# Kernel tuning notes

Hardware: AMD Instinct MI355X
Metric: run time of the kernel (lower is better)

Reference implementation:

```python
import jax, jax.numpy as jnp
import numpy as np

N_NODES = 10000
N_EDGES = 320000
H = 256
L = 3
EPS = 1e-5


def _mlp2(x, w1, b1, w2, b2):
    # Linear -> ReLU -> Linear
    return jax.nn.relu(x @ w1 + b1) @ w2 + b2


def _layer_norm(x, g, b):
    mu = jnp.mean(x, axis=-1, keepdims=True)
    var = jnp.var(x, axis=-1, keepdims=True)
    return (x - mu) * jax.lax.rsqrt(var + EPS) * g + b


def setup_inputs() -> dict:
    key = jax.random.key(0)
    ks = jax.random.split(key, 24)
    s = 0.02
    inp = {
        "node_features": jax.random.normal(ks[0], (N_NODES, H), dtype=jnp.float32),
        "edge_index": jax.random.randint(ks[1], (2, N_EDGES), 0, N_NODES, dtype=jnp.int64),
        # node encoder (Linear 256->256, ReLU, Linear 256->256)
        "ne_w1": jax.random.normal(ks[2], (H, H), dtype=jnp.float32) * s,
        "ne_b1": jnp.zeros((H,), jnp.float32),
        "ne_w2": jax.random.normal(ks[3], (H, H), dtype=jnp.float32) * s,
        "ne_b2": jnp.zeros((H,), jnp.float32),
        # per-layer message MLP (2H->H, ReLU, H->H), stacked over L layers
        "msg_w1": jax.random.normal(ks[4], (L, 2 * H, H), dtype=jnp.float32) * s,
        "msg_b1": jnp.zeros((L, H), jnp.float32),
        "msg_w2": jax.random.normal(ks[5], (L, H, H), dtype=jnp.float32) * s,
        "msg_b2": jnp.zeros((L, H), jnp.float32),
        # per-layer update MLP (2H->H, ReLU, H->H)
        "upd_w1": jax.random.normal(ks[6], (L, 2 * H, H), dtype=jnp.float32) * s,
        "upd_b1": jnp.zeros((L, H), jnp.float32),
        "upd_w2": jax.random.normal(ks[7], (L, H, H), dtype=jnp.float32) * s,
        "upd_b2": jnp.zeros((L, H), jnp.float32),
        # per-layer LayerNorm
        "ln_g": jnp.ones((L, H), jnp.float32),
        "ln_b": jnp.zeros((L, H), jnp.float32),
        # readout MLP
        "ro_w1": jax.random.normal(ks[8], (H, H), dtype=jnp.float32) * s,
        "ro_b1": jnp.zeros((H,), jnp.float32),
        "ro_w2": jax.random.normal(ks[9], (H, H), dtype=jnp.float32) * s,
        "ro_b2": jnp.zeros((H,), jnp.float32),
    }
    return inp


def reference(node_features, edge_index, ne_w1, ne_b1, ne_w2, ne_b2,
              msg_w1, msg_b1, msg_w2, msg_b2,
              upd_w1, upd_b1, upd_w2, upd_b2,
              ln_g, ln_b, ro_w1, ro_b1, ro_w2, ro_b2):
    n_nodes = node_features.shape[0]
    src, dst = edge_index[0], edge_index[1]

    # node encoder
    x = _mlp2(node_features, ne_w1, ne_b1, ne_w2, ne_b2)  # [N, H]

    # message passing layers (edge_attr is unused in the original layer)
    for l in range(L):
        cat_e = jnp.concatenate([x[src], x[dst]], axis=-1)          # [E, 2H]
        messages = _mlp2(cat_e, msg_w1[l], msg_b1[l], msg_w2[l], msg_b2[l])  # [E, H]
        aggregated = jax.ops.segment_sum(messages, dst, num_segments=n_nodes)  # [N, H]
        cat_n = jnp.concatenate([x, aggregated], axis=-1)           # [N, 2H]
        updated = _mlp2(cat_n, upd_w1[l], upd_b1[l], upd_w2[l], upd_b2[l])
        x = _layer_norm(x + updated, ln_g[l], ln_b[l])

    # mean readout
    g = jnp.mean(x, axis=0)  # [H]
    return _mlp2(g, ro_w1, ro_b1, ro_w2, ro_b2)  # [H]
```

## Files before the change

### kernel.cpp

```cpp
#include <hip/hip_runtime.h>

#define NN 10000
#define NE 320000
#define HD 256
#define NL 3

typedef unsigned short ushort_t;
typedef __attribute__((ext_vector_type(8))) short bf16x8;
typedef __attribute__((ext_vector_type(4))) float f32x4;

#define MFMA __builtin_amdgcn_mfma_f32_16x16x32_bf16

#define LGKMBAR() do { asm volatile("s_waitcnt lgkmcnt(0)" ::: "memory"); \
                       __builtin_amdgcn_s_barrier(); __builtin_amdgcn_sched_barrier(0); } while (0)

__device__ __forceinline__ unsigned short f2bf(float x) {
    unsigned u = __float_as_uint(x);
    unsigned rounding = 0x7FFFu + ((u >> 16) & 1u);
    return (unsigned short)((u + rounding) >> 16);
}
__device__ __forceinline__ float bf2f(unsigned short u) {
    return __uint_as_float(((unsigned)u) << 16);
}


__global__ void hist_deg(const int* __restrict__ dst, int* __restrict__ deg, int E) {
    int e = blockIdx.x * blockDim.x + threadIdx.x;
    if (e < E) atomicAdd(&deg[dst[e]], 1);
}

__global__ __launch_bounds__(1024) void scan_csr(const int* __restrict__ deg,
                                                 int* __restrict__ row_start,
                                                 int* __restrict__ cursor,
                                                 float* __restrict__ degf,
                                                 float* __restrict__ gsum, int n) {
    __shared__ int wsum[16];
    __shared__ int carry_s;
    int tid = threadIdx.x, lane = tid & 63, wid = tid >> 6;
    if (tid < HD) gsum[tid] = 0.f;
    if (tid == 0) carry_s = 0;
    __syncthreads();
    for (int base = 0; base < n; base += 1024) {
        int i = base + tid;
        int v = (i < n) ? deg[i] : 0;
        int s = v;
        #pragma unroll
        for (int off = 1; off < 64; off <<= 1) {
            int t = __shfl_up(s, off);
            if (lane >= off) s += t;
        }
        if (lane == 63) wsum[wid] = s;
        __syncthreads();
        if (wid == 0 && lane < 16) {
            int ws = wsum[lane];
            #pragma unroll
            for (int off = 1; off < 16; off <<= 1) {
                int t = __shfl_up(ws, off);
                if (lane >= off) ws += t;
            }
            wsum[lane] = ws;
        }
        __syncthreads();
        int carry = carry_s;
        int wpre = (wid > 0) ? wsum[wid - 1] : 0;
        int incl = carry + wpre + s;
        int excl = incl - v;
        if (i < n) { row_start[i] = excl; cursor[i] = excl; degf[i] = (float)v; }
        __syncthreads();
        if (tid == 1023) carry_s = incl;
        __syncthreads();
    }
    if (tid == 0) row_start[n] = carry_s;
}

__global__ void scatter_src(const int* __restrict__ src, const int* __restrict__ dst,
                            int* __restrict__ cursor, int* __restrict__ src_sorted, int E) {
    int e = blockIdx.x * blockDim.x + threadIdx.x;
    if (e < E) {
        int pos = atomicAdd(&cursor[dst[e]], 1);
        src_sorted[pos] = src[e];
    }
}


struct TDesc { const float* src; ushort_t* dst; int mode; };
struct TArgs { TDesc d[20]; };

__global__ __launch_bounds__(256) void conv_t(TArgs args) {
    __shared__ ushort_t tile[64][65];
    const float* src = args.d[blockIdx.y].src;
    ushort_t* dst = args.d[blockIdx.y].dst;
    int mode = args.d[blockIdx.y].mode;
    int t = blockIdx.x;
    int r0 = (t >> 2) * 64, c0 = (t & 3) * 64;
    int tid = threadIdx.x;
    int rr = tid >> 4, cc4 = (tid & 15) * 4;
    if (mode == 0) {
        #pragma unroll
        for (int i = 0; i < 4; ++i) {
            int r = r0 + rr + i * 16;
            float4 v = *(const float4*)(src + (size_t)r * HD + c0 + cc4);
            ushort4 o = { f2bf(v.x), f2bf(v.y), f2bf(v.z), f2bf(v.w) };
            *(ushort4*)(dst + (size_t)r * HD + c0 + cc4) = o;
        }
        return;
    }
    #pragma unroll
    for (int i = 0; i < 4; ++i) {
        int r = rr + i * 16;
        float4 v = *(const float4*)(src + (size_t)(r0 + r) * HD + c0 + cc4);
        tile[cc4 + 0][r] = f2bf(v.x);
        tile[cc4 + 1][r] = f2bf(v.y);
        tile[cc4 + 2][r] = f2bf(v.z);
        tile[cc4 + 3][r] = f2bf(v.w);
    }
    __syncthreads();
    #pragma unroll
    for (int i = 0; i < 4; ++i) {
        int c = rr + i * 16;
        ushort4 o = { tile[c][cc4], tile[c][cc4 + 1], tile[c][cc4 + 2], tile[c][cc4 + 3] };
        if (mode == 1) {
            *(ushort4*)(dst + (size_t)(c0 + c) * HD + r0 + cc4) = o;
        } else {
            int col = c0 + c;
            int k = r0 + cc4;
            *(ushort4*)(dst + (size_t)(k >> 5) * 8192 + col * 32 + (k & 31)) = o;
        }
    }
}

__global__ __launch_bounds__(256) void cast_nf_tiled(const float* __restrict__ src,
                                                     ushort_t* __restrict__ dst) {
    int blk = blockIdx.x;
    int row = threadIdx.x >> 4, g = threadIdx.x & 15;
    const float* sp = src + ((size_t)blk * 16 + row) * HD + g * 16;
    ushort_t* dp = dst + (size_t)blk * 4096 + (g >> 1) * 512 + row * 32 + (g & 1) * 16;
    #pragma unroll
    for (int j = 0; j < 4; ++j) {
        float4 v = *(const float4*)(sp + j * 4);
        ushort4 o = { f2bf(v.x), f2bf(v.y), f2bf(v.z), f2bf(v.w) };
        *(ushort4*)(dp + j * 4) = o;
    }
}

__global__ __launch_bounds__(256) void bias_compose(const float* __restrict__ mb2,
                                                    const float* __restrict__ uw1,
                                                    float* __restrict__ out) {
    int l = blockIdx.x, c = threadIdx.x;
    const float* b2l = mb2 + (size_t)l * HD;
    const float* u1b = uw1 + (size_t)l * 2 * HD * HD + (size_t)HD * HD;
    float s = 0.f;
    for (int k = 0; k < HD; ++k) s += b2l[k] * u1b[(size_t)k * HD + c];
    out[(size_t)l * HD + c] = s;
}

__global__ __launch_bounds__(256) void gemm_w2u(
    const ushort_t* __restrict__ Abase, const ushort_t* __restrict__ Btbase,
    ushort_t* __restrict__ outBase)
{
    const ushort_t* A  = Abase  + (size_t)blockIdx.z * HD * HD;
    const ushort_t* Bt = Btbase + (size_t)blockIdx.z * HD * HD;
    ushort_t* outB     = outBase + (size_t)blockIdx.z * HD * HD;
    int tid = threadIdx.x;
    int wid = tid >> 6, lane = tid & 63;
    int wm = wid >> 1, wn = wid & 1;
    int row0 = blockIdx.x * 64 + wm * 32;
    int col0 = blockIdx.y * 64 + wn * 32;
    int lm = lane & 15, lk = (lane >> 4) * 8;
    f32x4 acc[2][2] = {};
    const ushort_t* a0p = A + (size_t)(row0 + lm) * HD + lk;
    const ushort_t* a1p = A + (size_t)(row0 + 16 + lm) * HD + lk;
    const ushort_t* b0p = Bt + (size_t)(col0 + lm) * HD + lk;
    const ushort_t* b1p = Bt + (size_t)(col0 + 16 + lm) * HD + lk;
    #pragma unroll
    for (int k0 = 0; k0 < HD; k0 += 32) {
        bf16x8 a0 = *(const bf16x8*)(a0p + k0);
        bf16x8 a1 = *(const bf16x8*)(a1p + k0);
        bf16x8 b0 = *(const bf16x8*)(b0p + k0);
        bf16x8 b1 = *(const bf16x8*)(b1p + k0);
        acc[0][0] = MFMA(a0, b0, acc[0][0], 0, 0, 0);
        acc[0][1] = MFMA(a0, b1, acc[0][1], 0, 0, 0);
        acc[1][0] = MFMA(a1, b0, acc[1][0], 0, 0, 0);
        acc[1][1] = MFMA(a1, b1, acc[1][1], 0, 0, 0);
    }
    int orow = (lane >> 4) * 4;
    #pragma unroll
    for (int mi = 0; mi < 2; ++mi)
        #pragma unroll
        for (int r = 0; r < 4; ++r) {
            int row = row0 + mi * 16 + orow + r;
            #pragma unroll
            for (int ni = 0; ni < 2; ++ni) {
                int col = col0 + ni * 16 + lm;
                outB[(size_t)(col >> 5) * 8192 + row * 32 + (col & 31)] = f2bf(acc[mi][ni][r]);
            }
        }
}

__device__ __forceinline__ int swz(int row, int byte_in_row) {
    return row * 512 + (byte_in_row ^ ((row & 7) << 4));
}


__global__ __launch_bounds__(512, 4) void enc_pq(
    const ushort_t* __restrict__ Anf, const ushort_t* __restrict__ B1t,
    const ushort_t* __restrict__ B2t,
    const float* __restrict__ b1, const float* __restrict__ b2,
    const ushort_t* __restrict__ Pw1t, const ushort_t* __restrict__ Pw1b,
    const float* __restrict__ pqb1,
    float* __restrict__ xF, ushort_t* __restrict__ xB,
    ushort_t* __restrict__ P, float* __restrict__ Q, int M)
{
    __shared__ char hid[16 * 512];
    int tid = threadIdx.x;
    int w = tid >> 6, lane = tid & 63;
    int lm = lane & 15, q = lane >> 4;
    int row0 = blockIdx.x * 16;
    int col0 = w * 32;
    int cA = col0 + lm, cB = col0 + 16 + lm;
    size_t boff = (size_t)(col0 + lm) * 64 + q * 16;

    auto ldW = [&](const ushort_t* Wt, int s, int ni) -> bf16x8 {
        return *(const bf16x8*)((const char*)Wt + (size_t)s * 16384 + boff + ni * 1024);
    };
    const ushort_t* ap = Anf + (size_t)blockIdx.x * 4096 + lm * 32 + q * 8;

    bf16x8 wb[2][2], axr[2];
    #pragma unroll
    for (int s = 0; s < 2; ++s) {
        wb[s][0] = ldW(B1t, s, 0); wb[s][1] = ldW(B1t, s, 1);
        axr[s] = *(const bf16x8*)(ap + s * 512);
    }
    float b1v[2] = { b1[cA], b1[cB] };
    float b2v[2] = { b2[cA], b2[cB] };

    f32x4 acc[2] = {};
    #pragma unroll
    for (int j = 0; j < 8; ++j) {
        int p = j & 1;
        acc[0] = MFMA(axr[p], wb[p][0], acc[0], 0, 0, 0);
        acc[1] = MFMA(axr[p], wb[p][1], acc[1], 0, 0, 0);
        if (j < 6) {
            wb[p][0] = ldW(B1t, j + 2, 0); wb[p][1] = ldW(B1t, j + 2, 1);
            axr[p] = *(const bf16x8*)(ap + (j + 2) * 512);
        }
    }

    bf16x8 vw[2][2];
    #pragma unroll
    for (int s = 0; s < 2; ++s) { vw[s][0] = ldW(B2t, s, 0); vw[s][1] = ldW(B2t, s, 1); }

    #pragma unroll
    for (int ni = 0; ni < 2; ++ni) {
        int col = col0 + 16 * ni + lm;
        #pragma unroll
        for (int r = 0; r < 4; ++r) {
            int row = 4 * q + r;
            float v = fmaxf(acc[ni][r] + b1v[ni], 0.f);
            *(ushort_t*)(hid + swz(row, col * 2)) = f2bf(v);
        }
    }
    LGKMBAR();

    f32x4 acc2[2] = {};
    #pragma unroll
    for (int j = 0; j < 8; ++j) {
        int p = j & 1;
        int bk = (j * 32 + q * 8) * 2;
        bf16x8 a = *(const bf16x8*)(hid + swz(lm, bk));
        acc2[0] = MFMA(a, vw[p][0], acc2[0], 0, 0, 0);
        acc2[1] = MFMA(a, vw[p][1], acc2[1], 0, 0, 0);
        if (j < 6) { vw[p][0] = ldW(B2t, j + 2, 0); vw[p][1] = ldW(B2t, j + 2, 1); }
    }

    bf16x8 pw[2][2], qw[2][2];
    #pragma unroll
    for (int s = 0; s < 2; ++s) {
        pw[s][0] = ldW(Pw1t, s, 0); pw[s][1] = ldW(Pw1t, s, 1);
        qw[s][0] = ldW(Pw1b, s, 0); qw[s][1] = ldW(Pw1b, s, 1);
    }
    float pqv[2] = { pqb1[cA], pqb1[cB] };
    LGKMBAR();
    int tbase = blockIdx.x * 4096 + w * 512;
    #pragma unroll
    for (int ni = 0; ni < 2; ++ni) {
        int col = col0 + 16 * ni + lm;
        #pragma unroll
        for (int r = 0; r < 4; ++r) {
            int row = 4 * q + r;
            int grow = row0 + row;
            float v = acc2[ni][r] + b2v[ni];
            *(ushort_t*)(hid + swz(row, col * 2)) = f2bf(v);
            xF[(size_t)grow * HD + col] = v;
            xB[tbase + row * 32 + 16 * ni + lm] = f2bf(v);
        }
    }
    LGKMBAR();

    f32x4 aP[2] = {}, aQ[2] = {};
    #pragma unroll
    for (int j = 0; j < 8; ++j) {
        int p = j & 1;
        int bk = (j * 32 + q * 8) * 2;
        bf16x8 a = *(const bf16x8*)(hid + swz(lm, bk));
        aP[0] = MFMA(a, pw[p][0], aP[0], 0, 0, 0);
        aP[1] = MFMA(a, pw[p][1], aP[1], 0, 0, 0);
        aQ[0] = MFMA(a, qw[p][0], aQ[0], 0, 0, 0);
        aQ[1] = MFMA(a, qw[p][1], aQ[1], 0, 0, 0);
        if (j < 6) {
            pw[p][0] = ldW(Pw1t, j + 2, 0); pw[p][1] = ldW(Pw1t, j + 2, 1);
            qw[p][0] = ldW(Pw1b, j + 2, 0); qw[p][1] = ldW(Pw1b, j + 2, 1);
        }
    }
    #pragma unroll
    for (int r = 0; r < 4; ++r) {
        int grow = row0 + 4 * q + r;
        #pragma unroll
        for (int ni = 0; ni < 2; ++ni) {
            int col = col0 + 16 * ni + lm;
            P[(size_t)grow * HD + col] = f2bf(aP[ni][r]);
            Q[(size_t)grow * HD + col] = aQ[ni][r] + pqv[ni];
        }
    }
}


__global__ __launch_bounds__(256) void edge_agg(
    const ushort_t* __restrict__ Pb, const float* __restrict__ Qf,
    const int* __restrict__ row_start, const int* __restrict__ srcs,
    ushort_t* __restrict__ HaggT)
{
    int node = blockIdx.x * 4 + (threadIdx.x >> 6);
    int lane = threadIdx.x & 63;
    int c4 = lane * 4;
    float4 qb = *(const float4*)(Qf + (size_t)node * HD + c4);
    float4 acc = {0.f, 0.f, 0.f, 0.f};
    int j = row_start[node], e = row_start[node + 1];
    for (; j + 8 <= e; j += 8) {
        ushort4 p[8];
        #pragma unroll
        for (int u = 0; u < 8; ++u) {
            int s = srcs[j + u];
            p[u] = *(const ushort4*)(Pb + (size_t)s * HD + c4);
        }
        #pragma unroll
        for (int u = 0; u < 8; ++u) {
            acc.x += fmaxf(bf2f(p[u].x) + qb.x, 0.f);
            acc.y += fmaxf(bf2f(p[u].y) + qb.y, 0.f);
            acc.z += fmaxf(bf2f(p[u].z) + qb.z, 0.f);
            acc.w += fmaxf(bf2f(p[u].w) + qb.w, 0.f);
        }
    }
    for (; j < e; ++j) {
        int s0 = srcs[j];
        ushort4 p0 = *(const ushort4*)(Pb + (size_t)s0 * HD + c4);
        acc.x += fmaxf(bf2f(p0.x) + qb.x, 0.f);
        acc.y += fmaxf(bf2f(p0.y) + qb.y, 0.f);
        acc.z += fmaxf(bf2f(p0.z) + qb.z, 0.f);
        acc.w += fmaxf(bf2f(p0.w) + qb.w, 0.f);
    }
    ushort4 o = { f2bf(acc.x), f2bf(acc.y), f2bf(acc.z), f2bf(acc.w) };
    int tidx = (node >> 4) * 4096 + (c4 >> 5) * 512 + (node & 15) * 32 + (c4 & 31);
    *(ushort4*)(HaggT + tidx) = o;
}


__global__ __launch_bounds__(512, 4) void upd_ln(
    const ushort_t* __restrict__ xb, const ushort_t* __restrict__ Hb,
    const ushort_t* __restrict__ B1t, const ushort_t* __restrict__ B2t,
    const ushort_t* __restrict__ B3t,
    const float* __restrict__ degf,
    const float* __restrict__ b1, const float* __restrict__ bias2,
    const float* __restrict__ b3,
    const float* __restrict__ g, const float* __restrict__ bb,
    const ushort_t* __restrict__ Pw1t, const ushort_t* __restrict__ Pw1b,
    const float* __restrict__ pqb1,
    float* __restrict__ gsum,
    float* __restrict__ xF, ushort_t* __restrict__ xB,
    ushort_t* __restrict__ P, float* __restrict__ Q, int M)
{
    __shared__ char hid[16 * 512];
    __shared__ float sS[8][16], sQ[8][16], muv[16], ivv[16];
    int tid = threadIdx.x;
    int w = tid >> 6, lane = tid & 63;
    int lm = lane & 15, q = lane >> 4;
    int row0 = blockIdx.x * 16;
    int col0 = w * 32;
    int cA = col0 + lm, cB = col0 + 16 + lm;
    size_t boff = (size_t)(col0 + lm) * 64 + q * 16;

    auto ldW = [&](const ushort_t* Wt, int s, int ni) -> bf16x8 {
        return *(const bf16x8*)((const char*)Wt + (size_t)s * 16384 + boff + ni * 1024);
    };
    const ushort_t* xp = xb + (size_t)blockIdx.x * 4096 + lm * 32 + q * 8;
    const ushort_t* hp = Hb + (size_t)blockIdx.x * 4096 + lm * 32 + q * 8;

    bf16x8 wb[2][2][2], axr[2], ahr[2];
    #pragma unroll
    for (int s = 0; s < 2; ++s) {
        wb[s][0][0] = ldW(B1t, s, 0); wb[s][0][1] = ldW(B1t, s, 1);
        wb[s][1][0] = ldW(B2t, s, 0); wb[s][1][1] = ldW(B2t, s, 1);
        axr[s] = *(const bf16x8*)(xp + s * 512);
        ahr[s] = *(const bf16x8*)(hp + s * 512);
    }
    float b1v[2] = { b1[cA], b1[cB] };
    float bzv[2] = { bias2[cA], bias2[cB] };
    float dgv[4];
    #pragma unroll
    for (int r = 0; r < 4; ++r) dgv[r] = degf[min(row0 + 4 * q + r, M - 1)];

    f32x4 acc[2] = {};
    #pragma unroll
    for (int j = 0; j < 8; ++j) {
        int p = j & 1;
        acc[0] = MFMA(axr[p], wb[p][0][0], acc[0], 0, 0, 0);
        acc[0] = MFMA(ahr[p], wb[p][1][0], acc[0], 0, 0, 0);
        acc[1] = MFMA(axr[p], wb[p][0][1], acc[1], 0, 0, 0);
        acc[1] = MFMA(ahr[p], wb[p][1][1], acc[1], 0, 0, 0);
        if (j < 6) {
            wb[p][0][0] = ldW(B1t, j + 2, 0); wb[p][0][1] = ldW(B1t, j + 2, 1);
            wb[p][1][0] = ldW(B2t, j + 2, 0); wb[p][1][1] = ldW(B2t, j + 2, 1);
            axr[p] = *(const bf16x8*)(xp + (j + 2) * 512);
            ahr[p] = *(const bf16x8*)(hp + (j + 2) * 512);
        }
    }

    bf16x8 uw[2][2];
    #pragma unroll
    for (int s = 0; s < 2; ++s) { uw[s][0] = ldW(B3t, s, 0); uw[s][1] = ldW(B3t, s, 1); }

    #pragma unroll
    for (int r = 0; r < 4; ++r) {
        int row = 4 * q + r;
        #pragma unroll
        for (int ni = 0; ni < 2; ++ni) {
            int col = col0 + 16 * ni + lm;
            float v = fmaxf(acc[ni][r] + b1v[ni] + dgv[r] * bzv[ni], 0.f);
            *(ushort_t*)(hid + swz(row, col * 2)) = f2bf(v);
        }
    }
    LGKMBAR();

    float b3v[2] = { b3[cA], b3[cB] };
    float gv[2]  = { g[cA],  g[cB]  };
    float bbv[2] = { bb[cA], bb[cB] };
    float res[2][4];
    #pragma unroll
    for (int r = 0; r < 4; ++r) {
        int gr = min(row0 + 4 * q + r, M - 1);
        res[0][r] = xF[(size_t)gr * HD + cA];
        res[1][r] = xF[(size_t)gr * HD + cB];
    }

    f32x4 acc2[2] = {};
    #pragma unroll
    for (int j = 0; j < 8; ++j) {
        int p = j & 1;
        int bk = (j * 32 + q * 8) * 2;
        bf16x8 a = *(const bf16x8*)(hid + swz(lm, bk));
        acc2[0] = MFMA(a, uw[p][0], acc2[0], 0, 0, 0);
        acc2[1] = MFMA(a, uw[p][1], acc2[1], 0, 0, 0);
        if (j < 6) { uw[p][0] = ldW(B3t, j + 2, 0); uw[p][1] = ldW(B3t, j + 2, 1); }
    }

    bf16x8 pw[2][2], qw[2][2];
    float pqv[2] = { 0.f, 0.f };
    if (Pw1t) {
        #pragma unroll
        for (int s = 0; s < 2; ++s) {
            pw[s][0] = ldW(Pw1t, s, 0); pw[s][1] = ldW(Pw1t, s, 1);
            qw[s][0] = ldW(Pw1b, s, 0); qw[s][1] = ldW(Pw1b, s, 1);
        }
        pqv[0] = pqb1[cA]; pqv[1] = pqb1[cB];
    }

    #pragma unroll
    for (int r = 0; r < 4; ++r) {
        float s = 0.f, qq = 0.f;
        #pragma unroll
        for (int ni = 0; ni < 2; ++ni) {
            float v = acc2[ni][r] + b3v[ni] + res[ni][r];
            acc2[ni][r] = v;
            s += v; qq += v * v;
        }
        #pragma unroll
        for (int off = 1; off < 16; off <<= 1) {
            s += __shfl_xor(s, off);
            qq += __shfl_xor(qq, off);
        }
        if (lm == 0) {
            int row = 4 * q + r;
            sS[w][row] = s; sQ[w][row] = qq;
        }
    }
    LGKMBAR();
    if (tid < 16) {
        float s = 0.f, qq = 0.f;
        #pragma unroll
        for (int i = 0; i < 8; ++i) { s += sS[i][tid]; qq += sQ[i][tid]; }
        float mu = s * (1.0f / HD);
        float var = qq * (1.0f / HD) - mu * mu;
        muv[tid] = mu;
        ivv[tid] = rsqrtf(var + 1e-5f);
    }
    LGKMBAR();
    float csum[2] = {0.f, 0.f};
    int tbase = blockIdx.x * 4096 + w * 512;
    #pragma unroll
    for (int r = 0; r < 4; ++r) {
        int row = 4 * q + r;
        int grow = row0 + row;
        float mu = muv[row], iv = ivv[row];
        #pragma unroll
        for (int ni = 0; ni < 2; ++ni) {
            int col = col0 + 16 * ni + lm;
            float o = (acc2[ni][r] - mu) * iv * gv[ni] + bbv[ni];
            *(ushort_t*)(hid + swz(row, col * 2)) = f2bf(o);
            xF[(size_t)grow * HD + col] = o;
            xB[tbase + row * 32 + 16 * ni + lm] = f2bf(o);
            csum[ni] += o;
        }
    }
    if (gsum) {
        #pragma unroll
        for (int ni = 0; ni < 2; ++ni) {
            float s = csum[ni];
            s += __shfl_xor(s, 16);
            s += __shfl_xor(s, 32);
            if (q == 0) atomicAdd(&gsum[col0 + 16 * ni + lm], s);
        }
    }

    if (Pw1t) {
        LGKMBAR();
        f32x4 aP[2] = {}, aQ[2] = {};
        #pragma unroll
        for (int j = 0; j < 8; ++j) {
            int p = j & 1;
            int bk = (j * 32 + q * 8) * 2;
            bf16x8 a = *(const bf16x8*)(hid + swz(lm, bk));
            aP[0] = MFMA(a, pw[p][0], aP[0], 0, 0, 0);
            aP[1] = MFMA(a, pw[p][1], aP[1], 0, 0, 0);
            aQ[0] = MFMA(a, qw[p][0], aQ[0], 0, 0, 0);
            aQ[1] = MFMA(a, qw[p][1], aQ[1], 0, 0, 0);
            if (j < 6) {
                pw[p][0] = ldW(Pw1t, j + 2, 0); pw[p][1] = ldW(Pw1t, j + 2, 1);
                qw[p][0] = ldW(Pw1b, j + 2, 0); qw[p][1] = ldW(Pw1b, j + 2, 1);
            }
        }
        #pragma unroll
        for (int r = 0; r < 4; ++r) {
            int grow = row0 + 4 * q + r;
            #pragma unroll
            for (int ni = 0; ni < 2; ++ni) {
                int col = col0 + 16 * ni + lm;
                P[(size_t)grow * HD + col] = f2bf(aP[ni][r]);
                Q[(size_t)grow * HD + col] = aQ[ni][r] + pqv[ni];
            }
        }
    }
}


__global__ __launch_bounds__(256) void readout_mlp(
    const float* __restrict__ gsum,
    const float* __restrict__ w1, const float* __restrict__ b1,
    const float* __restrict__ w2, const float* __restrict__ b2,
    float* __restrict__ out, float invn)
{
    __shared__ float gl[HD], h1[HD];
    int c = threadIdx.x;
    gl[c] = gsum[c] * invn;
    __syncthreads();
    float a = b1[c];
    for (int k = 0; k < HD; ++k) a += gl[k] * w1[k * HD + c];
    h1[c] = fmaxf(a, 0.f);
    __syncthreads();
    float o = b2[c];
    for (int k = 0; k < HD; ++k) o += h1[k] * w2[k * HD + c];
    out[c] = o;
}


extern "C" void kernel_launch(void* const* d_in, const int* in_sizes, int n_in,
                              void* d_out, int out_size, void* d_ws, size_t ws_size,
                              hipStream_t stream) {
    const float* nf    = (const float*)d_in[0];
    const int*   ei    = (const int*)d_in[1];
    const float* ne_w1 = (const float*)d_in[2];
    const float* ne_b1 = (const float*)d_in[3];
    const float* ne_w2 = (const float*)d_in[4];
    const float* ne_b2 = (const float*)d_in[5];
    const float* mw1   = (const float*)d_in[6];
    const float* mb1   = (const float*)d_in[7];
    const float* mw2   = (const float*)d_in[8];
    const float* mb2   = (const float*)d_in[9];
    const float* uw1   = (const float*)d_in[10];
    const float* ub1   = (const float*)d_in[11];
    const float* uw2   = (const float*)d_in[12];
    const float* ub2   = (const float*)d_in[13];
    const float* lng   = (const float*)d_in[14];
    const float* lnb   = (const float*)d_in[15];
    const float* rw1   = (const float*)d_in[16];
    const float* rb1   = (const float*)d_in[17];
    const float* rw2   = (const float*)d_in[18];
    const float* rb2   = (const float*)d_in[19];

    const int* e_src = ei;
    const int* e_dst = ei + NE;

    char* w = (char*)d_ws;
    size_t off = 0;
    auto alloc = [&](size_t bytes) -> void* {
        void* p = w + off;
        off = (off + bytes + 255) & ~(size_t)255;
        return p;
    };
    const size_t NF32 = (size_t)NN * HD * sizeof(float);
    const size_t NF16 = (size_t)NN * HD * sizeof(ushort_t);
    const size_t WM16 = (size_t)HD * HD * sizeof(ushort_t);

    float* x    = (float*)alloc(NF32);
    float* Qf   = (float*)alloc(NF32);
    float* gsum = (float*)alloc(HD * sizeof(float));
    float* degf = (float*)alloc(NN * sizeof(float));
    float* b2u1 = (float*)alloc(NL * HD * sizeof(float));

    ushort_t* nfT   = (ushort_t*)alloc(NF16);
    ushort_t* xb    = (ushort_t*)alloc(NF16);
    ushort_t* Pb    = (ushort_t*)alloc(NF16);
    ushort_t* Haggb = (ushort_t*)alloc(NF16);
    ushort_t* neT1  = (ushort_t*)alloc(WM16);
    ushort_t* neT2  = (ushort_t*)alloc(WM16);
    ushort_t* w1tT  = (ushort_t*)alloc(NL * WM16);
    ushort_t* w1bT  = (ushort_t*)alloc(NL * WM16);
    ushort_t* u1tT  = (ushort_t*)alloc(NL * WM16);
    ushort_t* u1bT  = (ushort_t*)alloc(NL * WM16);
    ushort_t* u2T   = (ushort_t*)alloc(NL * WM16);
    ushort_t* w2uT  = (ushort_t*)alloc(NL * WM16);
    ushort_t* w2rmb = (ushort_t*)alloc(NL * WM16);

    int* deg       = (int*)alloc(NN * sizeof(int));
    int* row_start = (int*)alloc((NN + 1) * sizeof(int));
    int* cursor    = (int*)alloc(NN * sizeof(int));
    int* srcs      = (int*)alloc(NE * sizeof(int));

    hipMemsetAsync(deg, 0, NN * sizeof(int), stream);

    hist_deg<<<(NE + 255) / 256, 256, 0, stream>>>(e_dst, deg, NE);
    scan_csr<<<1, 1024, 0, stream>>>(deg, row_start, cursor, degf, gsum, NN);
    scatter_src<<<(NE + 255) / 256, 256, 0, stream>>>(e_src, e_dst, cursor, srcs, NE);

    TArgs ta;
    ta.d[0] = { ne_w1, neT1, 2 };
    ta.d[1] = { ne_w2, neT2, 2 };
    for (int l = 0; l < NL; ++l) {
        const float* w1l = mw1 + (size_t)l * 2 * HD * HD;
        const float* u1l = uw1 + (size_t)l * 2 * HD * HD;
        ta.d[2 + l]  = { w1l,                       w1tT + (size_t)l * HD * HD, 2 };
        ta.d[5 + l]  = { w1l + (size_t)HD * HD,     w1bT + (size_t)l * HD * HD, 2 };
        ta.d[8 + l]  = { u1l,                       u1tT + (size_t)l * HD * HD, 2 };
        ta.d[11 + l] = { u1l + (size_t)HD * HD,     u1bT + (size_t)l * HD * HD, 1 };
        ta.d[14 + l] = { uw2 + (size_t)l * HD * HD, u2T + (size_t)l * HD * HD, 2 };
        ta.d[17 + l] = { mw2 + (size_t)l * HD * HD, w2rmb + (size_t)l * HD * HD, 0 };
    }
    conv_t<<<dim3(16, 20), 256, 0, stream>>>(ta);
    cast_nf_tiled<<<NN / 16, 256, 0, stream>>>(nf, nfT);
    bias_compose<<<NL, 256, 0, stream>>>(mb2, uw1, b2u1);
    gemm_w2u<<<dim3(4, 4, NL), 256, 0, stream>>>(u1bT, w2rmb, w2uT);

    enc_pq<<<NN / 16, 512, 0, stream>>>(nfT, neT1, neT2, ne_b1, ne_b2,
                                        w1tT, w1bT, mb1, x, xb, Pb, Qf, NN);

    for (int l = 0; l < NL; ++l) {
        edge_agg<<<NN / 4, 256, 0, stream>>>(Pb, Qf, row_start, srcs, Haggb);
        int nl = l + 1;
        const ushort_t* pw1t = (nl < NL) ? w1tT + (size_t)nl * HD * HD : nullptr;
        const ushort_t* pw1b = (nl < NL) ? w1bT + (size_t)nl * HD * HD : nullptr;
        const float*    pqb1 = (nl < NL) ? mb1 + (size_t)nl * HD : nullptr;
        float* gs = (l == NL - 1) ? gsum : nullptr;
        upd_ln<<<NN / 16, 512, 0, stream>>>(
            xb, Haggb, u1tT + (size_t)l * HD * HD, w2uT + (size_t)l * HD * HD,
            u2T + (size_t)l * HD * HD, degf,
            ub1 + (size_t)l * HD, b2u1 + (size_t)l * HD, ub2 + (size_t)l * HD,
            lng + (size_t)l * HD, lnb + (size_t)l * HD,
            pw1t, pw1b, pqb1, gs, x, xb, Pb, Qf, NN);
    }

    readout_mlp<<<1, 256, 0, stream>>>(gsum, rw1, rb1, rw2, rb2, (float*)d_out, 1.0f / NN);
}
```

Measured before the change: 307.2 us.

## Fuse edge aggregation gather into update kernel with double-buffered P

Removes the separate edge_agg kernel. Each wave of upd_ln now gathers and reduces the messages for two of its block's 16 nodes and writes the bf16 result straight into a shared-memory tile, which then feeds the update GEMM. The P buffer is double-buffered across layers because other blocks still read the old P while this block writes the new one. This saves one launch per layer and the global write and read of the aggregated tensor. In exchange, the latency-bound gather now runs inside a register-heavy 512-thread kernel with fewer blocks in flight.

```diff
diff --git a/kernel.cpp b/kernel.cpp
--- a/kernel.cpp
+++ b/kernel.cpp
@@ -11,6 +11,7 @@
 
 #define MFMA __builtin_amdgcn_mfma_f32_16x16x32_bf16
 
+#define SCHEDPIN() __builtin_amdgcn_sched_barrier(0)
 #define LGKMBAR() do { asm volatile("s_waitcnt lgkmcnt(0)" ::: "memory"); \
                        __builtin_amdgcn_s_barrier(); __builtin_amdgcn_sched_barrier(0); } while (0)
 
@@ -325,48 +326,10 @@
 }
 
 
-__global__ __launch_bounds__(256) void edge_agg(
-    const ushort_t* __restrict__ Pb, const float* __restrict__ Qf,
+__global__ __launch_bounds__(512, 4) void upd_ln(
+    const ushort_t* __restrict__ xb,
+    const ushort_t* __restrict__ Pin, float* __restrict__ Qf,
     const int* __restrict__ row_start, const int* __restrict__ srcs,
-    ushort_t* __restrict__ HaggT)
-{
-    int node = blockIdx.x * 4 + (threadIdx.x >> 6);
-    int lane = threadIdx.x & 63;
-    int c4 = lane * 4;
-    float4 qb = *(const float4*)(Qf + (size_t)node * HD + c4);
-    float4 acc = {0.f, 0.f, 0.f, 0.f};
-    int j = row_start[node], e = row_start[node + 1];
-    for (; j + 8 <= e; j += 8) {
-        ushort4 p[8];
-        #pragma unroll
-        for (int u = 0; u < 8; ++u) {
-            int s = srcs[j + u];
-            p[u] = *(const ushort4*)(Pb + (size_t)s * HD + c4);
-        }
-        #pragma unroll
-        for (int u = 0; u < 8; ++u) {
-            acc.x += fmaxf(bf2f(p[u].x) + qb.x, 0.f);
-            acc.y += fmaxf(bf2f(p[u].y) + qb.y, 0.f);
-            acc.z += fmaxf(bf2f(p[u].z) + qb.z, 0.f);
-            acc.w += fmaxf(bf2f(p[u].w) + qb.w, 0.f);
-        }
-    }
-    for (; j < e; ++j) {
-        int s0 = srcs[j];
-        ushort4 p0 = *(const ushort4*)(Pb + (size_t)s0 * HD + c4);
-        acc.x += fmaxf(bf2f(p0.x) + qb.x, 0.f);
-        acc.y += fmaxf(bf2f(p0.y) + qb.y, 0.f);
-        acc.z += fmaxf(bf2f(p0.z) + qb.z, 0.f);
-        acc.w += fmaxf(bf2f(p0.w) + qb.w, 0.f);
-    }
-    ushort4 o = { f2bf(acc.x), f2bf(acc.y), f2bf(acc.z), f2bf(acc.w) };
-    int tidx = (node >> 4) * 4096 + (c4 >> 5) * 512 + (node & 15) * 32 + (c4 & 31);
-    *(ushort4*)(HaggT + tidx) = o;
-}
-
-
-__global__ __launch_bounds__(512, 4) void upd_ln(
-    const ushort_t* __restrict__ xb, const ushort_t* __restrict__ Hb,
     const ushort_t* __restrict__ B1t, const ushort_t* __restrict__ B2t,
     const ushort_t* __restrict__ B3t,
     const float* __restrict__ degf,
@@ -377,8 +340,9 @@
     const float* __restrict__ pqb1,
     float* __restrict__ gsum,
     float* __restrict__ xF, ushort_t* __restrict__ xB,
-    ushort_t* __restrict__ P, float* __restrict__ Q, int M)
+    ushort_t* __restrict__ Pout, int M)
 {
+    __shared__ char hag[8 * 1024];
     __shared__ char hid[16 * 512];
     __shared__ float sS[8][16], sQ[8][16], muv[16], ivv[16];
     int tid = threadIdx.x;
@@ -393,35 +357,70 @@
         return *(const bf16x8*)((const char*)Wt + (size_t)s * 16384 + boff + ni * 1024);
     };
     const ushort_t* xp = xb + (size_t)blockIdx.x * 4096 + lm * 32 + q * 8;
-    const ushort_t* hp = Hb + (size_t)blockIdx.x * 4096 + lm * 32 + q * 8;
-
-    bf16x8 wb[2][2][2], axr[2], ahr[2];
+
+    bf16x8 wb[2][2][2], axr[2];
     #pragma unroll
     for (int s = 0; s < 2; ++s) {
         wb[s][0][0] = ldW(B1t, s, 0); wb[s][0][1] = ldW(B1t, s, 1);
         wb[s][1][0] = ldW(B2t, s, 0); wb[s][1][1] = ldW(B2t, s, 1);
         axr[s] = *(const bf16x8*)(xp + s * 512);
-        ahr[s] = *(const bf16x8*)(hp + s * 512);
+    }
+    SCHEDPIN();
+
+    int c4 = lane * 4;
+    #pragma unroll
+    for (int t = 0; t < 2; ++t) {
+        int lrow = 2 * w + t;
+        int node = row0 + lrow;
+        float4 qb = *(const float4*)(Qf + (size_t)node * HD + c4);
+        float4 a4 = {0.f, 0.f, 0.f, 0.f};
+        int j = row_start[node], e = row_start[node + 1];
+        for (; j + 8 <= e; j += 8) {
+            ushort4 pv[8];
+            #pragma unroll
+            for (int u = 0; u < 8; ++u) {
+                int s = srcs[j + u];
+                pv[u] = *(const ushort4*)(Pin + (size_t)s * HD + c4);
+            }
+            #pragma unroll
+            for (int u = 0; u < 8; ++u) {
+                a4.x += fmaxf(bf2f(pv[u].x) + qb.x, 0.f);
+                a4.y += fmaxf(bf2f(pv[u].y) + qb.y, 0.f);
+                a4.z += fmaxf(bf2f(pv[u].z) + qb.z, 0.f);
+                a4.w += fmaxf(bf2f(pv[u].w) + qb.w, 0.f);
+            }
+        }
+        for (; j < e; ++j) {
+            int s = srcs[j];
+            ushort4 p0 = *(const ushort4*)(Pin + (size_t)s * HD + c4);
+            a4.x += fmaxf(bf2f(p0.x) + qb.x, 0.f);
+            a4.y += fmaxf(bf2f(p0.y) + qb.y, 0.f);
+            a4.z += fmaxf(bf2f(p0.z) + qb.z, 0.f);
+            a4.w += fmaxf(bf2f(p0.w) + qb.w, 0.f);
+        }
+        ushort4 o = { f2bf(a4.x), f2bf(a4.y), f2bf(a4.z), f2bf(a4.w) };
+        *(ushort4*)(hag + (c4 >> 5) * 1024 + lrow * 64 + (c4 & 31) * 2) = o;
     }
     float b1v[2] = { b1[cA], b1[cB] };
     float bzv[2] = { bias2[cA], bias2[cB] };
     float dgv[4];
     #pragma unroll
-    for (int r = 0; r < 4; ++r) dgv[r] = degf[min(row0 + 4 * q + r, M - 1)];
+    for (int r = 0; r < 4; ++r) dgv[r] = degf[row0 + 4 * q + r];
+    LGKMBAR();
 
     f32x4 acc[2] = {};
     #pragma unroll
     for (int j = 0; j < 8; ++j) {
         int p = j & 1;
+        bf16x8 ah = *(const bf16x8*)(hag + j * 1024 + lm * 64 + q * 16);
         acc[0] = MFMA(axr[p], wb[p][0][0], acc[0], 0, 0, 0);
-        acc[0] = MFMA(ahr[p], wb[p][1][0], acc[0], 0, 0, 0);
+        acc[0] = MFMA(ah, wb[p][1][0], acc[0], 0, 0, 0);
         acc[1] = MFMA(axr[p], wb[p][0][1], acc[1], 0, 0, 0);
-        acc[1] = MFMA(ahr[p], wb[p][1][1], acc[1], 0, 0, 0);
+        acc[1] = MFMA(ah, wb[p][1][1], acc[1], 0, 0, 0);
         if (j < 6) {
             wb[p][0][0] = ldW(B1t, j + 2, 0); wb[p][0][1] = ldW(B1t, j + 2, 1);
             wb[p][1][0] = ldW(B2t, j + 2, 0); wb[p][1][1] = ldW(B2t, j + 2, 1);
             axr[p] = *(const bf16x8*)(xp + (j + 2) * 512);
-            ahr[p] = *(const bf16x8*)(hp + (j + 2) * 512);
         }
     }
 
@@ -447,7 +446,7 @@
     float res[2][4];
     #pragma unroll
     for (int r = 0; r < 4; ++r) {
-        int gr = min(row0 + 4 * q + r, M - 1);
+        int gr = row0 + 4 * q + r;
         res[0][r] = xF[(size_t)gr * HD + cA];
         res[1][r] = xF[(size_t)gr * HD + cB];
     }
@@ -554,8 +553,8 @@
             #pragma unroll
             for (int ni = 0; ni < 2; ++ni) {
                 int col = col0 + 16 * ni + lm;
-                P[(size_t)grow * HD + col] = f2bf(aP[ni][r]);
-                Q[(size_t)grow * HD + col] = aQ[ni][r] + pqv[ni];
+                Pout[(size_t)grow * HD + col] = f2bf(aP[ni][r]);
+                Qf[(size_t)grow * HD + col] = aQ[ni][r] + pqv[ni];
             }
         }
     }
@@ -628,8 +627,8 @@
 
     ushort_t* nfT   = (ushort_t*)alloc(NF16);
     ushort_t* xb    = (ushort_t*)alloc(NF16);
-    ushort_t* Pb    = (ushort_t*)alloc(NF16);
-    ushort_t* Haggb = (ushort_t*)alloc(NF16);
+    ushort_t* PbA   = (ushort_t*)alloc(NF16);
+    ushort_t* PbB   = (ushort_t*)alloc(NF16);
     ushort_t* neT1  = (ushort_t*)alloc(WM16);
     ushort_t* neT2  = (ushort_t*)alloc(WM16);
     ushort_t* w1tT  = (ushort_t*)alloc(NL * WM16);
@@ -670,21 +669,24 @@
     gemm_w2u<<<dim3(4, 4, NL), 256, 0, stream>>>(u1bT, w2rmb, w2uT);
 
     enc_pq<<<NN / 16, 512, 0, stream>>>(nfT, neT1, neT2, ne_b1, ne_b2,
-                                        w1tT, w1bT, mb1, x, xb, Pb, Qf, NN);
-
+                                        w1tT, w1bT, mb1, x, xb, PbA, Qf, NN);
+
+    const ushort_t* pin = PbA;
+    ushort_t* pout = PbB;
     for (int l = 0; l < NL; ++l) {
-        edge_agg<<<NN / 4, 256, 0, stream>>>(Pb, Qf, row_start, srcs, Haggb);
         int nl = l + 1;
         const ushort_t* pw1t = (nl < NL) ? w1tT + (size_t)nl * HD * HD : nullptr;
         const ushort_t* pw1b = (nl < NL) ? w1bT + (size_t)nl * HD * HD : nullptr;
         const float*    pqb1 = (nl < NL) ? mb1 + (size_t)nl * HD : nullptr;
         float* gs = (l == NL - 1) ? gsum : nullptr;
         upd_ln<<<NN / 16, 512, 0, stream>>>(
-            xb, Haggb, u1tT + (size_t)l * HD * HD, w2uT + (size_t)l * HD * HD,
+            xb, pin, Qf, row_start, srcs,
+            u1tT + (size_t)l * HD * HD, w2uT + (size_t)l * HD * HD,
             u2T + (size_t)l * HD * HD, degf,
             ub1 + (size_t)l * HD, b2u1 + (size_t)l * HD, ub2 + (size_t)l * HD,
             lng + (size_t)l * HD, lnb + (size_t)l * HD,
-            pw1t, pw1b, pqb1, gs, x, xb, Pb, Qf, NN);
+            pw1t, pw1b, pqb1, gs, x, xb, pout, NN);
+        const ushort_t* tmp = pin; pin = pout; pout = (ushort_t*)tmp;
     }
 
     readout_mlp<<<1, 256, 0, stream>>>(gsum, rw1, rb1, rw2, rb2, (float*)d_out, 1.0f / NN);
```

New measurement: 314.0 us. 2.2% more time.
